# Optimization experiments

Hardware: AMD Instinct MI355X
Metric: run time of the kernel (lower is better)

Reference implementation:

```python
import jax, jax.numpy as jnp
import numpy as np

NUM_EMBEDDINGS = 4096
EMBEDDING_DIM = 256


def setup_inputs() -> dict:
    key = jax.random.key(0)
    k1, k2 = jax.random.split(key)
    # x: [B, C, H, W] latent feature map, C == embedding_dim
    x = jax.random.normal(k1, (4, EMBEDDING_DIM, 64, 64), dtype=jnp.float32)
    # codebook initialized uniform(-1/K, 1/K) as in the torch module
    emb = jax.random.uniform(
        k2, (NUM_EMBEDDINGS, EMBEDDING_DIM), dtype=jnp.float32,
        minval=-1.0 / NUM_EMBEDDINGS, maxval=1.0 / NUM_EMBEDDINGS)
    return {"x": x, "emb": emb}


def reference(x, emb):
    # x: [B, C, H, W] -> x_flat: [B, L, C] with L = H*W
    B, C = x.shape[0], x.shape[1]
    x_flat = x.reshape(B, C, -1).transpose(0, 2, 1)
    x_sq = jnp.sum(x_flat * x_flat, axis=2, keepdims=True)      # [B, L, 1]
    e_sq = jnp.sum(emb * emb, axis=1)                            # [K]
    dots = jnp.einsum('blc,kc->blk', x_flat, emb)                # [B, L, K]
    distances = x_sq + e_sq - 2.0 * dots
    closest_indices = jnp.argmin(distances, axis=2)              # [B, L]
    return closest_indices, distances
```

## Files before the change

kernel.cpp:

```cpp
#include <hip/hip_runtime.h>
#include <hip/hip_fp16.h>

#define BB 4
#define CC 256
#define LL 4096
#define MM 16384
#define KK 4096
#define MARGIN 1.0e-4f

typedef _Float16 half8 __attribute__((ext_vector_type(8)));
typedef _Float16 half4_ __attribute__((ext_vector_type(4)));
typedef float f32x4 __attribute__((ext_vector_type(4)));

#define GLOAD16(gp, lp) __builtin_amdgcn_global_load_lds( \
    (const __attribute__((address_space(1))) void*)(gp),  \
    (__attribute__((address_space(3))) void*)(lp), 16, 0, 0)

__global__ void vq_prep(const float* __restrict__ x, const float* __restrict__ emb,
                        _Float16* __restrict__ xh, float* __restrict__ xsq,
                        _Float16* __restrict__ eh, float* __restrict__ esq) {
  __shared__ float tl[32][260];
  const int t = threadIdx.x;
  if (blockIdx.x < 512) {
    const int b = blockIdx.x >> 7, l0 = (blockIdx.x & 127) * 32;
    const float* src = x + (size_t)b * CC * LL + l0;
#pragma unroll
    for (int it = 0; it < 32; ++it) {
      const int idx = it * 256 + t;
      const int c = idx >> 5, l = idx & 31;
      tl[l][c] = src[(size_t)c * LL + l];
    }
    __syncthreads();
#pragma unroll
    for (int it = 0; it < 4; ++it) {
      const int u = it * 256 + t;
      const int l = u >> 5, c8 = (u & 31) * 8;
      half8 h;
#pragma unroll
      for (int j = 0; j < 8; ++j) h[j] = (_Float16)tl[l][c8 + j];
      *(half8*)(xh + ((size_t)(b * LL + l0 + l)) * CC + c8) = h;
    }
    if (t < 32) {
      float S[2];
#pragma unroll
      for (int blk = 0; blk < 2; ++blk) {
        float v[16];
#pragma unroll
        for (int ln = 0; ln < 16; ++ln) {
          float q[8];
#pragma unroll
          for (int j = 0; j < 8; ++j) {
            const float xv = tl[t][blk * 128 + j * 16 + ln];
            q[j] = xv * xv;
          }
          v[ln] = ((q[0] + q[1]) + (q[2] + q[3])) + ((q[4] + q[5]) + (q[6] + q[7]));
        }
        float s1[8], s2[4], s3[2];
#pragma unroll
        for (int ln = 0; ln < 8; ++ln) s1[ln] = v[ln] + v[ln + 8];
#pragma unroll
        for (int ln = 0; ln < 4; ++ln) s2[ln] = s1[ln] + s1[ln + 4];
#pragma unroll
        for (int ln = 0; ln < 2; ++ln) s3[ln] = s2[ln] + s2[ln + 2];
        S[blk] = s3[0] + s3[1];
      }
      xsq[b * LL + l0 + t] = S[0] + S[1];
    }
  } else {
    const int lane = t & 63, w = t >> 6;
    const int q = (blockIdx.x - 512) * 4 + w;
    const float4 v = ((const float4*)(emb + (size_t)q * CC))[lane];
    float vv[4] = {v.x, v.y, v.z, v.w};
    _Float16 h[4];
#pragma unroll
    for (int i = 0; i < 4; ++i) h[i] = (_Float16)(vv[i] * 4096.0f);
    *(half4_*)(eh + (size_t)q * CC + lane * 4) = half4_{h[0], h[1], h[2], h[3]};
    if (lane == 0) {
      const float* pe = emb + (size_t)q * CC;
      float S[2];
#pragma unroll
      for (int blk = 0; blk < 2; ++blk) {
        float vt[16];
#pragma unroll
        for (int ln = 0; ln < 16; ++ln) {
          float qq[8];
#pragma unroll
          for (int j = 0; j < 8; ++j) {
            const float ev = pe[blk * 128 + j * 16 + ln];
            qq[j] = ev * ev;
          }
          vt[ln] = ((qq[0] + qq[1]) + (qq[2] + qq[3])) + ((qq[4] + qq[5]) + (qq[6] + qq[7]));
        }
        float s1[8], s2[4], s3[2];
#pragma unroll
        for (int ln = 0; ln < 8; ++ln) s1[ln] = vt[ln] + vt[ln + 8];
#pragma unroll
        for (int ln = 0; ln < 4; ++ln) s2[ln] = s1[ln] + s1[ln + 4];
#pragma unroll
        for (int ln = 0; ln < 2; ++ln) s3[ln] = s2[ln] + s2[ln + 2];
        S[blk] = s3[0] + s3[1];
      }
      esq[q] = S[0] + S[1];
    }
  }
}

__global__ __launch_bounds__(256) void vq_gemm(
    const _Float16* __restrict__ xh, const _Float16* __restrict__ eh,
    const float* __restrict__ xsq, const float* __restrict__ esq,
    float* __restrict__ out,
    float* __restrict__ ps1, int* __restrict__ pi1, float* __restrict__ ps2) {
  __shared__ __align__(16) char smem[32768];
  _Float16* sAb[2] = {(_Float16*)smem, (_Float16*)(smem + 16384)};
  _Float16* sBb[2] = {(_Float16*)(smem + 8192), (_Float16*)(smem + 24576)};
  float* sOut = (float*)smem;

  const int t = threadIdx.x, lane = t & 63, wid = t >> 6;
  const int wm = wid >> 1, wn = wid & 1;
  const int m0 = blockIdx.x * 128, n0 = blockIdx.y * 128;
  const int lm = lane & 15, kb = lane >> 4;

  const int srow = lane >> 2;
  const int scol = (lane & 3) * 8;
  const int chunk0 = wid * 2, chunk1 = wid * 2 + 1;
  const int row0 = chunk0 * 16 + srow, row1 = chunk1 * 16 + srow;

  float ev[4], xs4[4][4];
#pragma unroll
  for (int ni = 0; ni < 4; ++ni) ev[ni] = esq[n0 + wn * 64 + ni * 16 + lm];
#pragma unroll
  for (int mi = 0; mi < 4; ++mi)
#pragma unroll
    for (int r = 0; r < 4; ++r)
      xs4[mi][r] = xsq[m0 + wm * 64 + mi * 16 + kb * 4 + r];
  __builtin_amdgcn_sched_barrier(0);

#define STAGE(ks, buf) do {                                                   \
    const int kc_ = (ks) * 32 + scol;                                         \
    GLOAD16(xh + (size_t)(m0 + row0) * CC + kc_, sAb[buf] + chunk0 * 512);    \
    GLOAD16(eh + (size_t)(n0 + row0) * CC + kc_, sBb[buf] + chunk0 * 512);    \
    GLOAD16(xh + (size_t)(m0 + row1) * CC + kc_, sAb[buf] + chunk1 * 512);    \
    GLOAD16(eh + (size_t)(n0 + row1) * CC + kc_, sBb[buf] + chunk1 * 512);    \
  } while (0)

  f32x4 acc[4][4] = {};
  STAGE(0, 0);
#pragma unroll
  for (int ks = 0; ks < 8; ++ks) {
    const int cur = ks & 1;
    if (ks < 7) {
      STAGE(ks + 1, cur ^ 1);
      asm volatile("s_waitcnt vmcnt(4)" ::: "memory");
    } else {
      asm volatile("s_waitcnt vmcnt(0)" ::: "memory");
    }
    __builtin_amdgcn_s_barrier();
    __builtin_amdgcn_sched_barrier(0);

    half8 a[4], bfr[4];
#pragma unroll
    for (int i = 0; i < 4; ++i) {
      a[i]   = *(const half8*)&sAb[cur][(wm * 64 + i * 16 + lm) * 32 + kb * 8];
      bfr[i] = *(const half8*)&sBb[cur][(wn * 64 + i * 16 + lm) * 32 + kb * 8];
    }
#pragma unroll
    for (int mi = 0; mi < 4; ++mi)
#pragma unroll
      for (int ni = 0; ni < 4; ++ni)
        acc[mi][ni] = __builtin_amdgcn_mfma_f32_16x16x32_f16(a[mi], bfr[ni], acc[mi][ni], 0, 0, 0);

    if (ks < 7) {
      asm volatile("s_waitcnt lgkmcnt(0)" ::: "memory");
      __builtin_amdgcn_s_barrier();
      __builtin_amdgcn_sched_barrier(0);
    }
  }
#undef STAGE

#define EPI_BAR() do {                                          \
    asm volatile("s_waitcnt lgkmcnt(0)" ::: "memory");          \
    __builtin_amdgcn_s_barrier();                               \
    __builtin_amdgcn_sched_barrier(0);                          \
  } while (0)

  const int swz = kb << 4;
  const int erow = t >> 3, ej = t & 7;
  const int esw = ((erow >> 2) & 3) << 4;
  const int egm0 = m0 + (erow >> 4) * 64 + (erow & 15);

#pragma unroll
  for (int mi = 0; mi < 4; ++mi) {
#pragma unroll
    for (int r = 0; r < 4; ++r) {
      const int row = wm * 16 + kb * 4 + r;
#pragma unroll
      for (int ni = 0; ni < 4; ++ni) {
        float t1 = xs4[mi][r] + ev[ni];
        float d = t1 - acc[mi][ni][r] * 4.8828125e-4f;
        sOut[row * 128 + ((wn * 64 + ni * 16 + lm) ^ swz)] = d;
      }
    }
    EPI_BAR();
    float s1 = 3.4e38f, s2 = 3.4e38f;
    int q1 = 0x7fffffff;
    const int gm = egm0 + mi * 16;
#pragma unroll
    for (int i = 0; i < 4; ++i) {
      const int c = 4 * ej + 32 * i;
      const f32x4 v = *(const f32x4*)&sOut[erow * 128 + (c ^ esw)];
      __builtin_nontemporal_store(v, (f32x4*)(out + MM + (size_t)gm * (size_t)KK + n0 + c));
#pragma unroll
      for (int e = 0; e < 4; ++e) {
        const float d = v[e];
        const int q = n0 + c + e;
        if (d < s1 || (d == s1 && q < q1)) { s2 = s1; s1 = d; q1 = q; }
        else s2 = fminf(s2, d);
      }
    }
#pragma unroll
    for (int off = 1; off < 8; off <<= 1) {
      float o1 = __shfl_xor(s1, off), o2 = __shfl_xor(s2, off);
      int oq = __shfl_xor(q1, off);
      float mx = fmaxf(s1, o1);
      if (o1 < s1 || (o1 == s1 && oq < q1)) { s1 = o1; q1 = oq; }
      s2 = fminf(fminf(s2, o2), mx);
    }
    if (ej == 0) {
      const size_t pidx = (size_t)gm * 32 + blockIdx.y;
      ps1[pidx] = s1; pi1[pidx] = q1; ps2[pidx] = s2;
    }
    if (mi < 3) EPI_BAR();
  }
#undef EPI_BAR
}

__global__ void vq_finish(const float* __restrict__ ps1, const int* __restrict__ pi1,
                          const float* __restrict__ ps2, const float* __restrict__ dist,
                          const float* __restrict__ x, const float* __restrict__ emb,
                          const float* __restrict__ xsq, const float* __restrict__ esq,
                          float* __restrict__ out) {
  __shared__ float xr[4][CC];
  __shared__ int cq[4][64];
  __shared__ int cnt[4];
  const int lane = threadIdx.x & 63, w = threadIdx.x >> 6;
  const int m = blockIdx.x * 4 + w;

  float s1 = 3.4e38f, s2 = 3.4e38f;
  int q1 = 0x7fffffff;
  if (lane < 32) {
    const size_t base = (size_t)m * 32 + lane;
    s1 = ps1[base]; s2 = ps2[base]; q1 = pi1[base];
  }
#pragma unroll
  for (int off = 1; off < 32; off <<= 1) {
    float o1 = __shfl_xor(s1, off), o2 = __shfl_xor(s2, off);
    int oq = __shfl_xor(q1, off);
    float mx = fmaxf(s1, o1);
    if (o1 < s1 || (o1 == s1 && oq < q1)) { s1 = o1; q1 = oq; }
    s2 = fminf(fminf(s2, o2), mx);
  }
  s1 = __shfl(s1, 0); s2 = __shfl(s2, 0); q1 = __shfl(q1, 0);

  if (s2 - s1 > MARGIN) {
    if (lane == 0) out[m] = (float)q1;
    return;
  }

  const int b = m >> 12, l = m & 4095;
#pragma unroll
  for (int j = 0; j < 4; ++j)
    xr[w][lane * 4 + j] = x[((size_t)b * CC + lane * 4 + j) * LL + l];
  if (lane == 0) cnt[w] = 0;

  const float thr = s1 + MARGIN;
  const float4* d4 = (const float4*)(dist + (size_t)m * KK);
  for (int i = 0; i < 16; ++i) {
    float4 v = d4[i * 64 + lane];
    float vv[4] = {v.x, v.y, v.z, v.w};
#pragma unroll
    for (int e = 0; e < 4; ++e)
      if (vv[e] <= thr) {
        int slot = atomicAdd(&cnt[w], 1);
        if (slot < 64) cq[w][slot] = (i * 64 + lane) * 4 + e;
      }
  }
  const int nc = min(cnt[w], 64);
  float bs = 3.4e38f;
  int bq = 0x7fffffff;
  if (lane < nc) {
    const int q = cq[w][lane];
    const float* e = emb + (size_t)q * CC;
    float a = 0.f;
    for (int c = 0; c < CC; ++c) a = fmaf(xr[w][c], e[c], a);
    float t1 = xsq[m] + esq[q];
    bs = t1 - 2.0f * a;
    bq = q;
  }
#pragma unroll
  for (int off = 1; off < 64; off <<= 1) {
    float os = __shfl_xor(bs, off);
    int oq = __shfl_xor(bq, off);
    if (os < bs || (os == bs && oq < bq)) { bs = os; bq = oq; }
  }
  if (lane == 0) out[m] = (float)bq;
}

extern "C" void kernel_launch(void* const* d_in, const int* in_sizes, int n_in,
                              void* d_out, int out_size, void* d_ws, size_t ws_size,
                              hipStream_t stream) {
  const float* x = (const float*)d_in[0];
  const float* emb = (const float*)d_in[1];
  float* out = (float*)d_out;
  char* ws = (char*)d_ws;

  _Float16* xh = (_Float16*)(ws + 0);
  _Float16* eh = (_Float16*)(ws + 8388608);
  float* xsq = (float*)(ws + 10485760);
  float* esq = (float*)(ws + 10551296);
  float* ps1 = (float*)(ws + 10567680);
  int*   pi1 = (int*)(ws + 12664832);
  float* ps2 = (float*)(ws + 14761984);

  vq_prep<<<1536, 256, 0, stream>>>(x, emb, xh, xsq, eh, esq);
  vq_gemm<<<dim3(128, 32), 256, 0, stream>>>(xh, eh, xsq, esq, out, ps1, pi1, ps2);
  vq_finish<<<4096, 256, 0, stream>>>(ps1, pi1, ps2, out + MM, x, emb, xsq, esq, out);
}
```

Measured before the change: 129.6 us.

## Widen GEMM block tile to 128x256 with 8 waves and halve partial reductions

The distance GEMM block now uses 512 threads with a 128x256 output tile, so each X tile loaded into LDS is reused across twice as many codebook columns. The epilogue is restructured into four 32-row chunks over 256-wide rows. The per-row partial argmin count drops from 32 to 16, which also shrinks the finish kernel's reduction. The trade-offs are more LDS per block (48KB), fewer blocks in the grid, and an extra barrier at the end of the k loop.

```diff
diff --git a/kernel.cpp b/kernel.cpp
--- a/kernel.cpp
+++ b/kernel.cpp
@@ -105,42 +105,36 @@
   }
 }
 
-__global__ __launch_bounds__(256) void vq_gemm(
+__global__ __launch_bounds__(512, 4) void vq_gemm(
     const _Float16* __restrict__ xh, const _Float16* __restrict__ eh,
     const float* __restrict__ xsq, const float* __restrict__ esq,
     float* __restrict__ out,
     float* __restrict__ ps1, int* __restrict__ pi1, float* __restrict__ ps2) {
-  __shared__ __align__(16) char smem[32768];
-  _Float16* sAb[2] = {(_Float16*)smem, (_Float16*)(smem + 16384)};
-  _Float16* sBb[2] = {(_Float16*)(smem + 8192), (_Float16*)(smem + 24576)};
+  __shared__ __align__(16) char smem[49152];
   float* sOut = (float*)smem;
 
   const int t = threadIdx.x, lane = t & 63, wid = t >> 6;
-  const int wm = wid >> 1, wn = wid & 1;
-  const int m0 = blockIdx.x * 128, n0 = blockIdx.y * 128;
+  const int wm = wid >> 2, wn = wid & 3;
+  const int m0 = blockIdx.x * 128, n0 = blockIdx.y * 256;
   const int lm = lane & 15, kb = lane >> 4;
 
   const int srow = lane >> 2;
   const int scol = (lane & 3) * 8;
-  const int chunk0 = wid * 2, chunk1 = wid * 2 + 1;
-  const int row0 = chunk0 * 16 + srow, row1 = chunk1 * 16 + srow;
-
-  float ev[4], xs4[4][4];
-#pragma unroll
-  for (int ni = 0; ni < 4; ++ni) ev[ni] = esq[n0 + wn * 64 + ni * 16 + lm];
-#pragma unroll
-  for (int mi = 0; mi < 4; ++mi)
-#pragma unroll
-    for (int r = 0; r < 4; ++r)
-      xs4[mi][r] = xsq[m0 + wm * 64 + mi * 16 + kb * 4 + r];
-  __builtin_amdgcn_sched_barrier(0);
-
+  const int c0 = wid * 3, c1 = wid * 3 + 1, c2 = wid * 3 + 2;
+
+#define SA(b) ((_Float16*)(smem + (b) * 24576))
+#define SB(b) ((_Float16*)(smem + (b) * 24576 + 8192))
+#define STAGE1(c, buf, kc_) do {                                              \
+    if ((c) < 8)                                                              \
+      GLOAD16(xh + (size_t)(m0 + (c) * 16 + srow) * CC + (kc_) + scol,        \
+              SA(buf) + (c) * 512);                                           \
+    else                                                                      \
+      GLOAD16(eh + (size_t)(n0 + ((c) - 8) * 16 + srow) * CC + (kc_) + scol,  \
+              SB(buf) + ((c) - 8) * 512);                                     \
+  } while (0)
 #define STAGE(ks, buf) do {                                                   \
-    const int kc_ = (ks) * 32 + scol;                                         \
-    GLOAD16(xh + (size_t)(m0 + row0) * CC + kc_, sAb[buf] + chunk0 * 512);    \
-    GLOAD16(eh + (size_t)(n0 + row0) * CC + kc_, sBb[buf] + chunk0 * 512);    \
-    GLOAD16(xh + (size_t)(m0 + row1) * CC + kc_, sAb[buf] + chunk1 * 512);    \
-    GLOAD16(eh + (size_t)(n0 + row1) * CC + kc_, sBb[buf] + chunk1 * 512);    \
+    const int kc_ = (ks) * 32;                                                \
+    STAGE1(c0, buf, kc_); STAGE1(c1, buf, kc_); STAGE1(c2, buf, kc_);         \
   } while (0)
 
   f32x4 acc[4][4] = {};
@@ -150,7 +144,7 @@
     const int cur = ks & 1;
     if (ks < 7) {
       STAGE(ks + 1, cur ^ 1);
-      asm volatile("s_waitcnt vmcnt(4)" ::: "memory");
+      asm volatile("s_waitcnt vmcnt(3)" ::: "memory");
     } else {
       asm volatile("s_waitcnt vmcnt(0)" ::: "memory");
     }
@@ -160,8 +154,8 @@
     half8 a[4], bfr[4];
 #pragma unroll
     for (int i = 0; i < 4; ++i) {
-      a[i]   = *(const half8*)&sAb[cur][(wm * 64 + i * 16 + lm) * 32 + kb * 8];
-      bfr[i] = *(const half8*)&sBb[cur][(wn * 64 + i * 16 + lm) * 32 + kb * 8];
+      a[i]   = *(const half8*)&SA(cur)[(wm * 64 + i * 16 + lm) * 32 + kb * 8];
+      bfr[i] = *(const half8*)&SB(cur)[(wn * 64 + i * 16 + lm) * 32 + kb * 8];
     }
 #pragma unroll
     for (int mi = 0; mi < 4; ++mi)
@@ -169,13 +163,21 @@
       for (int ni = 0; ni < 4; ++ni)
         acc[mi][ni] = __builtin_amdgcn_mfma_f32_16x16x32_f16(a[mi], bfr[ni], acc[mi][ni], 0, 0, 0);
 
-    if (ks < 7) {
-      asm volatile("s_waitcnt lgkmcnt(0)" ::: "memory");
-      __builtin_amdgcn_s_barrier();
-      __builtin_amdgcn_sched_barrier(0);
-    }
+    asm volatile("s_waitcnt lgkmcnt(0)" ::: "memory");
+    __builtin_amdgcn_s_barrier();
+    __builtin_amdgcn_sched_barrier(0);
   }
 #undef STAGE
+#undef STAGE1
+
+  float ev[4], xs4[4][4];
+#pragma unroll
+  for (int ni = 0; ni < 4; ++ni) ev[ni] = esq[n0 + wn * 64 + ni * 16 + lm];
+#pragma unroll
+  for (int mi = 0; mi < 4; ++mi)
+#pragma unroll
+    for (int r = 0; r < 4; ++r)
+      xs4[mi][r] = xsq[m0 + wm * 64 + mi * 16 + kb * 4 + r];
 
 #define EPI_BAR() do {                                          \
     asm volatile("s_waitcnt lgkmcnt(0)" ::: "memory");          \
@@ -184,30 +186,35 @@
   } while (0)
 
   const int swz = kb << 4;
-  const int erow = t >> 3, ej = t & 7;
+  const int erow = t >> 4, ej = t & 15;
   const int esw = ((erow >> 2) & 3) << 4;
-  const int egm0 = m0 + (erow >> 4) * 64 + (erow & 15);
-
-#pragma unroll
-  for (int mi = 0; mi < 4; ++mi) {
-#pragma unroll
-    for (int r = 0; r < 4; ++r) {
-      const int row = wm * 16 + kb * 4 + r;
-#pragma unroll
-      for (int ni = 0; ni < 4; ++ni) {
-        float t1 = xs4[mi][r] + ev[ni];
-        float d = t1 - acc[mi][ni][r] * 4.8828125e-4f;
-        sOut[row * 128 + ((wn * 64 + ni * 16 + lm) ^ swz)] = d;
+
+#pragma unroll
+  for (int ch = 0; ch < 4; ++ch) {
+    if (wm == (ch >> 1)) {
+#pragma unroll
+      for (int mh = 0; mh < 2; ++mh) {
+        const int mi = (ch & 1) * 2 + mh;
+        const int lrbase = mh * 16 + kb * 4;
+#pragma unroll
+        for (int r = 0; r < 4; ++r) {
+#pragma unroll
+          for (int ni = 0; ni < 4; ++ni) {
+            float t1 = xs4[mi][r] + ev[ni];
+            float d = t1 - acc[mi][ni][r] * 4.8828125e-4f;
+            sOut[(lrbase + r) * 256 + ((wn * 64 + ni * 16 + lm) ^ swz)] = d;
+          }
+        }
       }
     }
     EPI_BAR();
     float s1 = 3.4e38f, s2 = 3.4e38f;
     int q1 = 0x7fffffff;
-    const int gm = egm0 + mi * 16;
+    const int gm = m0 + ch * 32 + erow;
 #pragma unroll
     for (int i = 0; i < 4; ++i) {
-      const int c = 4 * ej + 32 * i;
-      const f32x4 v = *(const f32x4*)&sOut[erow * 128 + (c ^ esw)];
+      const int c = 4 * ej + 64 * i;
+      const f32x4 v = *(const f32x4*)&sOut[erow * 256 + (c ^ esw)];
       __builtin_nontemporal_store(v, (f32x4*)(out + MM + (size_t)gm * (size_t)KK + n0 + c));
 #pragma unroll
       for (int e = 0; e < 4; ++e) {
@@ -218,7 +225,7 @@
       }
     }
 #pragma unroll
-    for (int off = 1; off < 8; off <<= 1) {
+    for (int off = 1; off < 16; off <<= 1) {
       float o1 = __shfl_xor(s1, off), o2 = __shfl_xor(s2, off);
       int oq = __shfl_xor(q1, off);
       float mx = fmaxf(s1, o1);
@@ -226,12 +233,14 @@
       s2 = fminf(fminf(s2, o2), mx);
     }
     if (ej == 0) {
-      const size_t pidx = (size_t)gm * 32 + blockIdx.y;
+      const size_t pidx = (size_t)gm * 16 + blockIdx.y;
       ps1[pidx] = s1; pi1[pidx] = q1; ps2[pidx] = s2;
     }
-    if (mi < 3) EPI_BAR();
+    if (ch < 3) EPI_BAR();
   }
 #undef EPI_BAR
+#undef SA
+#undef SB
 }
 
 __global__ void vq_finish(const float* __restrict__ ps1, const int* __restrict__ pi1,
@@ -247,12 +256,12 @@
 
   float s1 = 3.4e38f, s2 = 3.4e38f;
   int q1 = 0x7fffffff;
-  if (lane < 32) {
-    const size_t base = (size_t)m * 32 + lane;
+  if (lane < 16) {
+    const size_t base = (size_t)m * 16 + lane;
     s1 = ps1[base]; s2 = ps2[base]; q1 = pi1[base];
   }
 #pragma unroll
-  for (int off = 1; off < 32; off <<= 1) {
+  for (int off = 1; off < 16; off <<= 1) {
     float o1 = __shfl_xor(s1, off), o2 = __shfl_xor(s2, off);
     int oq = __shfl_xor(q1, off);
     float mx = fmaxf(s1, o1);
@@ -318,10 +327,10 @@
   float* xsq = (float*)(ws + 10485760);
   float* esq = (float*)(ws + 10551296);
   float* ps1 = (float*)(ws + 10567680);
-  int*   pi1 = (int*)(ws + 12664832);
-  float* ps2 = (float*)(ws + 14761984);
+  int*   pi1 = (int*)(ws + 11616256);
+  float* ps2 = (float*)(ws + 12664832);
 
   vq_prep<<<1536, 256, 0, stream>>>(x, emb, xh, xsq, eh, esq);
-  vq_gemm<<<dim3(128, 32), 256, 0, stream>>>(xh, eh, xsq, esq, out, ps1, pi1, ps2);
+  vq_gemm<<<dim3(128, 16), 512, 0, stream>>>(xh, eh, xsq, esq, out, ps1, pi1, ps2);
   vq_finish<<<4096, 256, 0, stream>>>(ps1, pi1, ps2, out + MM, x, emb, xsq, esq, out);
 }
```

After: 192.5 us. 1.49x slower.
